# Kernel optimization log

Hardware: AMD Instinct MI355X
Metric: run time of the kernel (lower is better)

Reference implementation:

```python
import jax, jax.numpy as jnp
import numpy as np

TOP_K = 2


def setup_inputs() -> dict:
    key = jax.random.key(0)
    k1, k2, k3, k4 = jax.random.split(key, 4)
    B, S, D, F, E = 4, 512, 512, 2048, 16
    hidden_states = jax.random.normal(k1, (B, S, D), dtype=jnp.float32)
    gate_weight = jax.random.normal(k2, (E, D), dtype=jnp.float32) * 0.02
    w1 = jax.random.normal(k3, (E, F, D), dtype=jnp.float32) * 0.02
    w2 = jax.random.normal(k4, (E, D, F), dtype=jnp.float32) * 0.02
    return {"hidden_states": hidden_states, "gate_weight": gate_weight, "w1": w1, "w2": w2}


def reference(hidden_states, gate_weight, w1, w2):
    B, S, D = hidden_states.shape
    E = gate_weight.shape[0]
    x = hidden_states.reshape(-1, D)  # [T, D]

    # fused_top_k_routing: logits = x @ Wg^T, top-k, softmax over the k values
    gate_logits = x @ gate_weight.T  # [T, E]
    top_vals, top_idx = jax.lax.top_k(gate_logits, TOP_K)  # [T, k]
    routing_w = jax.nn.softmax(top_vals, axis=-1)  # [T, k]

    # _prepare_expert_inputs: token t goes to expert e iff e in its top-k
    mask = jnp.any(top_idx[:, :, None] == jnp.arange(E)[None, None, :], axis=1)  # [T, E] bool

    # Expert FFN on routed tokens, computed densely over (token, expert) pairs then masked.
    # h[t,e,f] = silu(x_t @ W1_e^T)
    h = jax.nn.silu(jnp.einsum('td,efd->tef', x, w1))  # [T, E, F]
    counts = jnp.sum(mask, axis=0)  # [E]
    h_sum = jnp.einsum('tef,te->ef', h, mask.astype(h.dtype))  # [E, F]
    h_mean = h_sum / jnp.maximum(counts, 1)[:, None].astype(h.dtype)

    # fused_expert_scatter_gather uses expert_outputs[e].mean(dim=0);
    # mean(W2 @ act) = W2 @ mean(act) since W2 is linear.
    y_mean = jnp.einsum('ef,edf->ed', h_mean, w2)  # [E, D]
    y_mean = jnp.where((counts > 0)[:, None], y_mean, 0.0)

    # per-token combine: sum_k w_k * mean_output[expert_k]
    out = jnp.einsum('tk,tkd->td', routing_w, y_mean[top_idx])  # [T, D]
    return out.reshape(B, S, D)
```

## Files before the change

### kernel.cpp

```cpp
#include <hip/hip_runtime.h>

#define NTOK   2048
#define DIM    512
#define FDIM   2048
#define NEXP   16
#define CAP    768
#define FT     32
#define TC     128

typedef __bf16 bf16x8 __attribute__((ext_vector_type(8)));
typedef __bf16 bf16x4 __attribute__((ext_vector_type(4)));
typedef float  floatx4 __attribute__((ext_vector_type(4)));

#define WS_COUNTS    0
#define WS_ZEROPAGE  1024
#define WS_TOPIDX    4096
#define WS_ROUTW     20480
#define WS_HMEAN     36864
#define WS_YMEAN     167936
#define WS_XG        200704
#define WS_ZERO_BYTES 2048

__device__ __forceinline__ void async_lds16(const void* g, void* l) {
    __builtin_amdgcn_global_load_lds(
        (__attribute__((address_space(1))) void*)(void*)g,
        (__attribute__((address_space(3))) void*)l, 16, 0, 0);
}

__global__ __launch_bounds__(256) void k1_route_gather(
    const float* __restrict__ x, const float* __restrict__ gw,
    int* __restrict__ counts, int* __restrict__ top_idx,
    float* __restrict__ routw, __bf16* __restrict__ Xg)
{
    __shared__ float xt[16 * DIM];
    __shared__ float lg[16][17];
    __shared__ int   gdst[16][2];
    const int tid = threadIdx.x;
    const int t0  = blockIdx.x * 16;

    {
        const float4* src = (const float4*)(x + (size_t)t0 * DIM);
        float4* dst = (float4*)xt;
        #pragma unroll
        for (int i = 0; i < 8; ++i) dst[i * 256 + tid] = src[i * 256 + tid];
    }
    __syncthreads();

    {
        const int tl = tid >> 4, e = tid & 15;
        const float4* xr = (const float4*)(xt + tl * DIM);
        const float4* gr = (const float4*)(gw + e * DIM);
        float acc = 0.f;
        #pragma unroll 8
        for (int j = 0; j < DIM / 4; ++j) {
            float4 a = xr[j], b = gr[j];
            acc += a.x * b.x + a.y * b.y + a.z * b.z + a.w * b.w;
        }
        lg[tl][e] = acc;
    }
    __syncthreads();

    if (tid < 16) {
        const int tl = tid;
        float v0 = -1e30f, v1 = -1e30f; int i0 = 0, i1 = 0;
        #pragma unroll
        for (int e = 0; e < NEXP; ++e) {
            float v = lg[tl][e];
            if (v > v0)      { v1 = v0; i1 = i0; v0 = v; i0 = e; }
            else if (v > v1) { v1 = v;  i1 = e; }
        }
        float e1 = __expf(v1 - v0);
        float w0 = 1.f / (1.f + e1);
        float w1 = 1.f - w0;
        const int t = t0 + tl;
        top_idx[t * 2]     = i0; top_idx[t * 2 + 1] = i1;
        routw[t * 2]       = w0; routw[t * 2 + 1]   = w1;
        int p0 = atomicAdd(counts + i0, 1);
        int p1 = atomicAdd(counts + i1, 1);
        gdst[tl][0] = (p0 < CAP) ? (i0 * CAP + p0) : -1;
        gdst[tl][1] = (p1 < CAP) ? (i1 * CAP + p1) : -1;
    }
    __syncthreads();

    #pragma unroll
    for (int it = 0; it < 16; ++it) {
        int s   = it * 256 + tid;
        int job = s >> 7, el = s & 127;
        int tl  = job >> 1, k = job & 1;
        int dst = gdst[tl][k];
        if (dst >= 0) {
            float4 v = ((const float4*)(xt + tl * DIM))[el];
            bf16x4 o = { (__bf16)v.x, (__bf16)v.y, (__bf16)v.z, (__bf16)v.w };
            *(bf16x4*)(Xg + (size_t)dst * DIM + el * 4) = o;
        }
    }
}

__global__ __launch_bounds__(256) void k2_expert_ffn(
    const float* __restrict__ w1, const __bf16* __restrict__ Xg,
    const int* __restrict__ counts, const __bf16* __restrict__ zp,
    float* __restrict__ hmean)
{
    __shared__ __align__(16) __bf16 w1s[64 * 33 * 8];
    __shared__ __align__(16) __bf16 xs[2][8 * 128 * 8];
    __shared__ float hred[FT][4];

    const int tid = threadIdx.x;
    const int bid = blockIdx.x;
    const int e   = ((bid & 7) << 1) | (bid >> 9);
    const int f0  = ((bid >> 3) & 63) * FT;
    const int cnt = min(counts[e], CAP);
    const float inv = 1.f / (float)max(cnt, 1);

    const int wv   = tid >> 6;
    const int lane = tid & 63;
    const int q    = lane >> 4;
    const int l15  = lane & 15;
    const int tsub = wv * 32;

    const int nchunk = (cnt + TC - 1) / TC;
    const int total  = nchunk * 8;

    auto STAGE = [&](int b, int tc, int c) {
        __bf16* dst0 = xs[b];
        #pragma unroll
        for (int it = 0; it < 4; ++it) {
            int base = it * 256 + wv * 64;
            int slot = base + lane;
            int kg = slot >> 7, t = slot & 127;
            int r  = tc * TC + t;
            const __bf16* src = (r < cnt)
                ? (Xg + ((size_t)(e * CAP + r)) * DIM + c * 64 + kg * 8)
                : zp;
            async_lds16(src, dst0 + (size_t)base * 8);
        }
    };

    if (total > 0) STAGE(0, 0, 0);

    #pragma unroll
    for (int it = 0; it < 8; ++it) {
        int s = it * 256 + tid;
        int kg = s & 63, f = s >> 6;
        const float* src = w1 + ((size_t)(e * FDIM + f0 + f)) * DIM + kg * 8;
        float4 a = ((const float4*)src)[0];
        float4 b = ((const float4*)src)[1];
        bf16x8 v;
        v[0] = (__bf16)a.x; v[1] = (__bf16)a.y; v[2] = (__bf16)a.z; v[3] = (__bf16)a.w;
        v[4] = (__bf16)b.x; v[5] = (__bf16)b.y; v[6] = (__bf16)b.z; v[7] = (__bf16)b.w;
        *(bf16x8*)(w1s + ((size_t)kg * 33 + f) * 8) = v;
    }
    __syncthreads();

    floatx4 acc[2][2];
    #pragma unroll
    for (int a = 0; a < 2; ++a)
        #pragma unroll
        for (int b = 0; b < 2; ++b) acc[a][b] = (floatx4)0.f;
    float rs[2][4] = {{0.f, 0.f, 0.f, 0.f}, {0.f, 0.f, 0.f, 0.f}};

    for (int g = 0; g < total; ++g) {
        const int cur = g & 1;
        const int c   = g & 7;
        if (g + 1 < total) STAGE(cur ^ 1, (g + 1) >> 3, (g + 1) & 7);

        const __bf16* xb = xs[cur];
        #pragma unroll
        for (int ks = 0; ks < 2; ++ks) {
            int kga = c * 8 + ks * 4 + q;
            int kl  = ks * 4 + q;
            bf16x8 a0 = *(const bf16x8*)(w1s + ((size_t)kga * 33 + l15) * 8);
            bf16x8 a1 = *(const bf16x8*)(w1s + ((size_t)kga * 33 + 16 + l15) * 8);
            bf16x8 b0 = *(const bf16x8*)(xb + ((size_t)kl * 128 + tsub + l15) * 8);
            bf16x8 b1 = *(const bf16x8*)(xb + ((size_t)kl * 128 + tsub + 16 + l15) * 8);
            acc[0][0] = __builtin_amdgcn_mfma_f32_16x16x32_bf16(a0, b0, acc[0][0], 0, 0, 0);
            acc[0][1] = __builtin_amdgcn_mfma_f32_16x16x32_bf16(a0, b1, acc[0][1], 0, 0, 0);
            acc[1][0] = __builtin_amdgcn_mfma_f32_16x16x32_bf16(a1, b0, acc[1][0], 0, 0, 0);
            acc[1][1] = __builtin_amdgcn_mfma_f32_16x16x32_bf16(a1, b1, acc[1][1], 0, 0, 0);
        }
        if (c == 7) {
            #pragma unroll
            for (int fa = 0; fa < 2; ++fa)
                #pragma unroll
                for (int r = 0; r < 4; ++r) {
                    float v0 = acc[fa][0][r], v1 = acc[fa][1][r];
                    rs[fa][r] += v0 / (1.f + __expf(-v0)) + v1 / (1.f + __expf(-v1));
                    acc[fa][0][r] = 0.f; acc[fa][1][r] = 0.f;
                }
        }
        __syncthreads();
    }

    #pragma unroll
    for (int fa = 0; fa < 2; ++fa)
        #pragma unroll
        for (int r = 0; r < 4; ++r) {
            float v = rs[fa][r];
            v += __shfl_xor(v, 1);
            v += __shfl_xor(v, 2);
            v += __shfl_xor(v, 4);
            v += __shfl_xor(v, 8);
            rs[fa][r] = v;
        }
    if (l15 == 0) {
        #pragma unroll
        for (int fa = 0; fa < 2; ++fa)
            #pragma unroll
            for (int r = 0; r < 4; ++r)
                hred[fa * 16 + q * 4 + r][wv] = rs[fa][r];
    }
    __syncthreads();
    if (tid < FT)
        hmean[(size_t)e * FDIM + f0 + tid] =
            (hred[tid][0] + hred[tid][1] + hred[tid][2] + hred[tid][3]) * inv;
}

__global__ __launch_bounds__(256) void k3_ymean(
    const float* __restrict__ w2, const float* __restrict__ hmean,
    const int* __restrict__ counts, float* __restrict__ ymean)
{
    __shared__ float hl[FDIM];
    const int tid = threadIdx.x;
    const int bid = blockIdx.x;
    const int e   = bid >> 7;
    const int d0  = (bid & 127) * 4;

    {
        const float4* hg = (const float4*)(hmean + (size_t)e * FDIM);
        float4* hl4 = (float4*)hl;
        hl4[tid]       = hg[tid];
        hl4[256 + tid] = hg[256 + tid];
    }
    __syncthreads();

    const int wv = tid >> 6, lane = tid & 63;
    const int d = d0 + wv;
    const float4* wr  = (const float4*)(w2 + ((size_t)e * DIM + d) * FDIM);
    const float4* hl4 = (const float4*)hl;
    float acc = 0.f;
    #pragma unroll
    for (int i = 0; i < 8; ++i) {
        float4 a = wr[i * 64 + lane];
        float4 h = hl4[i * 64 + lane];
        acc += a.x * h.x + a.y * h.y + a.z * h.z + a.w * h.w;
    }
    #pragma unroll
    for (int m = 1; m < 64; m <<= 1) acc += __shfl_xor(acc, m);
    if (lane == 0)
        ymean[e * DIM + d] = (counts[e] > 0) ? acc : 0.f;
}

__global__ __launch_bounds__(256) void k4_combine(
    const int* __restrict__ top_idx, const float* __restrict__ routw,
    const float* __restrict__ ymean, float* __restrict__ out)
{
    const int idx = blockIdx.x * 256 + threadIdx.x;
    const int t = idx >> 7;
    const int c = idx & 127;
    const int i0 = top_idx[t * 2], i1 = top_idx[t * 2 + 1];
    const float w0 = routw[t * 2], w1 = routw[t * 2 + 1];
    float4 a = ((const float4*)(ymean + (size_t)i0 * DIM))[c];
    float4 b = ((const float4*)(ymean + (size_t)i1 * DIM))[c];
    float4 o;
    o.x = w0 * a.x + w1 * b.x;
    o.y = w0 * a.y + w1 * b.y;
    o.z = w0 * a.z + w1 * b.z;
    o.w = w0 * a.w + w1 * b.w;
    ((float4*)out)[idx] = o;
}

extern "C" void kernel_launch(void* const* d_in, const int* in_sizes, int n_in,
                              void* d_out, int out_size, void* d_ws, size_t ws_size,
                              hipStream_t stream)
{
    (void)in_sizes; (void)n_in; (void)out_size; (void)ws_size;
    const float* x  = (const float*)d_in[0];
    const float* gw = (const float*)d_in[1];
    const float* w1 = (const float*)d_in[2];
    const float* w2 = (const float*)d_in[3];
    float* out = (float*)d_out;

    char* ws = (char*)d_ws;
    int*    counts  = (int*)   (ws + WS_COUNTS);
    const __bf16* zp = (const __bf16*)(ws + WS_ZEROPAGE);
    int*    top_idx = (int*)   (ws + WS_TOPIDX);
    float*  routw   = (float*) (ws + WS_ROUTW);
    float*  hmean   = (float*) (ws + WS_HMEAN);
    float*  ymean   = (float*) (ws + WS_YMEAN);
    __bf16* Xg      = (__bf16*)(ws + WS_XG);

    hipMemsetAsync(d_ws, 0, WS_ZERO_BYTES, stream);

    k1_route_gather<<<dim3(NTOK / 16), dim3(256), 0, stream>>>(x, gw, counts, top_idx, routw, Xg);
    k2_expert_ffn  <<<dim3(NEXP * (FDIM / FT)), dim3(256), 0, stream>>>(w1, Xg, counts, zp, hmean);
    k3_ymean       <<<dim3(NEXP * 128), dim3(256), 0, stream>>>(w2, hmean, counts, ymean);
    k4_combine     <<<dim3(NTOK * DIM / 4 / 256), dim3(256), 0, stream>>>(top_idx, routw, ymean, out);
}
```

Before: 234.3 us.

## Load routed tokens directly from global into registers, drop LDS staging

New measurement: 273.3 us. 16.7% more time.

```diff
diff --git a/kernel.cpp b/kernel.cpp
--- a/kernel.cpp
+++ b/kernel.cpp
@@ -6,7 +6,6 @@
 #define NEXP   16
 #define CAP    768
 #define FT     32
-#define TC     128
 
 typedef __bf16 bf16x8 __attribute__((ext_vector_type(8)));
 typedef __bf16 bf16x4 __attribute__((ext_vector_type(4)));
@@ -20,12 +19,6 @@
 #define WS_YMEAN     167936
 #define WS_XG        200704
 #define WS_ZERO_BYTES 2048
-
-__device__ __forceinline__ void async_lds16(const void* g, void* l) {
-    __builtin_amdgcn_global_load_lds(
-        (__attribute__((address_space(1))) void*)(void*)g,
-        (__attribute__((address_space(3))) void*)l, 16, 0, 0);
-}
 
 __global__ __launch_bounds__(256) void k1_route_gather(
     const float* __restrict__ x, const float* __restrict__ gw,
@@ -96,13 +89,12 @@
     }
 }
 
-__global__ __launch_bounds__(256) void k2_expert_ffn(
+__global__ __launch_bounds__(256, 4) void k2_expert_ffn(
     const float* __restrict__ w1, const __bf16* __restrict__ Xg,
     const int* __restrict__ counts, const __bf16* __restrict__ zp,
     float* __restrict__ hmean)
 {
     __shared__ __align__(16) __bf16 w1s[64 * 33 * 8];
-    __shared__ __align__(16) __bf16 xs[2][8 * 128 * 8];
     __shared__ float hred[FT][4];
 
     const int tid = threadIdx.x;
@@ -112,31 +104,10 @@
     const int cnt = min(counts[e], CAP);
     const float inv = 1.f / (float)max(cnt, 1);
 
-    const int wv   = tid >> 6;
+    const int wv  = tid >> 6;
     const int lane = tid & 63;
-    const int q    = lane >> 4;
-    const int l15  = lane & 15;
-    const int tsub = wv * 32;
-
-    const int nchunk = (cnt + TC - 1) / TC;
-    const int total  = nchunk * 8;
-
-    auto STAGE = [&](int b, int tc, int c) {
-        __bf16* dst0 = xs[b];
-        #pragma unroll
-        for (int it = 0; it < 4; ++it) {
-            int base = it * 256 + wv * 64;
-            int slot = base + lane;
-            int kg = slot >> 7, t = slot & 127;
-            int r  = tc * TC + t;
-            const __bf16* src = (r < cnt)
-                ? (Xg + ((size_t)(e * CAP + r)) * DIM + c * 64 + kg * 8)
-                : zp;
-            async_lds16(src, dst0 + (size_t)base * 8);
-        }
-    };
-
-    if (total > 0) STAGE(0, 0, 0);
+    const int q   = lane >> 4;
+    const int l15 = lane & 15;
 
     #pragma unroll
     for (int it = 0; it < 8; ++it) {
@@ -152,43 +123,69 @@
     }
     __syncthreads();
 
-    floatx4 acc[2][2];
-    #pragma unroll
-    for (int a = 0; a < 2; ++a)
-        #pragma unroll
-        for (int b = 0; b < 2; ++b) acc[a][b] = (floatx4)0.f;
+    const __bf16* xbase = Xg + (size_t)e * CAP * DIM + q * 8;
+    const __bf16* pz    = zp + q * 8;
+
     float rs[2][4] = {{0.f, 0.f, 0.f, 0.f}, {0.f, 0.f, 0.f, 0.f}};
-
-    for (int g = 0; g < total; ++g) {
-        const int cur = g & 1;
-        const int c   = g & 7;
-        if (g + 1 < total) STAGE(cur ^ 1, (g + 1) >> 3, (g + 1) & 7);
-
-        const __bf16* xb = xs[cur];
-        #pragma unroll
-        for (int ks = 0; ks < 2; ++ks) {
-            int kga = c * 8 + ks * 4 + q;
-            int kl  = ks * 4 + q;
-            bf16x8 a0 = *(const bf16x8*)(w1s + ((size_t)kga * 33 + l15) * 8);
-            bf16x8 a1 = *(const bf16x8*)(w1s + ((size_t)kga * 33 + 16 + l15) * 8);
-            bf16x8 b0 = *(const bf16x8*)(xb + ((size_t)kl * 128 + tsub + l15) * 8);
-            bf16x8 b1 = *(const bf16x8*)(xb + ((size_t)kl * 128 + tsub + 16 + l15) * 8);
-            acc[0][0] = __builtin_amdgcn_mfma_f32_16x16x32_bf16(a0, b0, acc[0][0], 0, 0, 0);
-            acc[0][1] = __builtin_amdgcn_mfma_f32_16x16x32_bf16(a0, b1, acc[0][1], 0, 0, 0);
-            acc[1][0] = __builtin_amdgcn_mfma_f32_16x16x32_bf16(a1, b0, acc[1][0], 0, 0, 0);
-            acc[1][1] = __builtin_amdgcn_mfma_f32_16x16x32_bf16(a1, b1, acc[1][1], 0, 0, 0);
-        }
-        if (c == 7) {
+    const int nsc = (cnt + 255) >> 8;
+
+    for (int sc = 0; sc < nsc; ++sc) {
+        floatx4 acc[2][2][2];
+        #pragma unroll
+        for (int h = 0; h < 2; ++h)
+            #pragma unroll
+            for (int a = 0; a < 2; ++a)
+                #pragma unroll
+                for (int b = 0; b < 2; ++b) acc[h][a][b] = (floatx4)0.f;
+
+        const int b00 = sc * 256 + wv * 32;
+        const __bf16* p[2][2];
+        #pragma unroll
+        for (int h = 0; h < 2; ++h)
+            #pragma unroll
+            for (int tt = 0; tt < 2; ++tt) {
+                int r = b00 + h * 128 + tt * 16 + l15;
+                p[h][tt] = (r < cnt) ? (xbase + (size_t)r * DIM) : pz;
+            }
+        const bool h1 = (b00 + 128) < cnt;
+
+        #pragma unroll
+        for (int c = 0; c < 8; ++c) {
+            bf16x8 A[2][2];
+            #pragma unroll
+            for (int ks = 0; ks < 2; ++ks)
+                #pragma unroll
+                for (int fa = 0; fa < 2; ++fa)
+                    A[ks][fa] = *(const bf16x8*)(
+                        w1s + ((size_t)((c * 8 + ks * 4 + q) * 33) + fa * 16 + l15) * 8);
+            #pragma unroll
+            for (int ks = 0; ks < 2; ++ks) {
+                const int off = (c * 8 + ks * 4) * 8;
+                bf16x8 b0 = *(const bf16x8*)(p[0][0] + off);
+                bf16x8 b1 = *(const bf16x8*)(p[0][1] + off);
+                acc[0][0][0] = __builtin_amdgcn_mfma_f32_16x16x32_bf16(A[ks][0], b0, acc[0][0][0], 0, 0, 0);
+                acc[0][0][1] = __builtin_amdgcn_mfma_f32_16x16x32_bf16(A[ks][0], b1, acc[0][0][1], 0, 0, 0);
+                acc[0][1][0] = __builtin_amdgcn_mfma_f32_16x16x32_bf16(A[ks][1], b0, acc[0][1][0], 0, 0, 0);
+                acc[0][1][1] = __builtin_amdgcn_mfma_f32_16x16x32_bf16(A[ks][1], b1, acc[0][1][1], 0, 0, 0);
+                if (h1) {
+                    bf16x8 c0 = *(const bf16x8*)(p[1][0] + off);
+                    bf16x8 c1 = *(const bf16x8*)(p[1][1] + off);
+                    acc[1][0][0] = __builtin_amdgcn_mfma_f32_16x16x32_bf16(A[ks][0], c0, acc[1][0][0], 0, 0, 0);
+                    acc[1][0][1] = __builtin_amdgcn_mfma_f32_16x16x32_bf16(A[ks][0], c1, acc[1][0][1], 0, 0, 0);
+                    acc[1][1][0] = __builtin_amdgcn_mfma_f32_16x16x32_bf16(A[ks][1], c0, acc[1][1][0], 0, 0, 0);
+                    acc[1][1][1] = __builtin_amdgcn_mfma_f32_16x16x32_bf16(A[ks][1], c1, acc[1][1][1], 0, 0, 0);
+                }
+            }
+        }
+        #pragma unroll
+        for (int h = 0; h < 2; ++h)
             #pragma unroll
             for (int fa = 0; fa < 2; ++fa)
                 #pragma unroll
                 for (int r = 0; r < 4; ++r) {
-                    float v0 = acc[fa][0][r], v1 = acc[fa][1][r];
+                    float v0 = acc[h][fa][0][r], v1 = acc[h][fa][1][r];
                     rs[fa][r] += v0 / (1.f + __expf(-v0)) + v1 / (1.f + __expf(-v1));
-                    acc[fa][0][r] = 0.f; acc[fa][1][r] = 0.f;
                 }
-        }
-        __syncthreads();
     }
 
     #pragma unroll
```
